# Kernel tuning notes

Measured on AMD Instinct MI355X. Metric: run time of the kernel, lower is better.

The kernel has to match this reference:

```python
import math
import jax, jax.numpy as jnp
import numpy as np

B, K, D, R = 8192, 64, 128, 8
EPSILON = 1.0  # alpha_scale, used as diffusion epsilon


def setup_inputs() -> dict:
    key = jax.random.key(0)
    k1, k2, k3 = jax.random.split(key, 3)
    y = jax.random.normal(k1, (B, D), dtype=jnp.float32)
    m = 0.2 * jax.random.normal(k2, (K, D), dtype=jnp.float32)          # init_mean_scale=0.2
    delta = jnp.full((K, D), -2.0, dtype=jnp.float32)                    # init_delta=-2.0
    U = 0.001 * jax.random.normal(k3, (K, D, R), dtype=jnp.float32)
    # log_alpha_raw = alpha_scale * log(ones(K)/K)
    log_alpha_raw = jnp.full((K,), math.log(1.0 / K), dtype=jnp.float32)
    return {"y": y, "m": m, "delta": delta, "U": U, "log_alpha_raw": log_alpha_raw}


def reference(y, m, delta, U, log_alpha_raw):
    """log z_theta(y) = logsumexp_k [log_alpha_k + log N(y; m_k, eps*S_k)],
    S_k = diag(exp(delta_k)) + U_k U_k^T, solved via Woodbury + Cholesky."""
    d = y.shape[-1]
    eps = jnp.asarray(EPSILON, y.dtype)
    log_alpha = (log_alpha_raw - jnp.mean(log_alpha_raw)) / EPSILON

    S_diag = jnp.exp(delta)            # [K, d]
    S_inv = 1.0 / S_diag               # [K, d]

    # Capacitance M_k = I_r + U_k^T diag(S_inv_k) U_k, Cholesky L_k
    V = S_inv[..., None] * U                              # [K, d, r]
    Mcap = jnp.eye(R, dtype=y.dtype) + jnp.einsum('kdr,kds->krs', U, V)  # [K, r, r]
    L = jnp.linalg.cholesky(Mcap)                         # [K, r, r]
    logdet_S = jnp.sum(jnp.log(S_diag), axis=-1) \
        + 2.0 * jnp.sum(jnp.log(jnp.diagonal(L, axis1=-2, axis2=-1)), axis=-1)  # [K]

    diff = y[:, None, :] - m[None, :, :]                  # [B, K, d]
    u1 = diff * S_inv[None]                               # [B, K, d]
    # Woodbury correction: solve M_k s = U_k^T u1 for all (b, k)
    t = jnp.einsum('kdr,bkd->krb', U, u1)                 # [K, r, B] (B as multiple RHS)
    z1 = jax.scipy.linalg.solve_triangular(L, t, lower=True)
    s = jax.scipy.linalg.solve_triangular(jnp.swapaxes(L, -1, -2), z1, lower=False)  # [K, r, B]
    Us = jnp.einsum('kdr,krb->bkd', U, s)                 # [B, K, d]
    S_inv_diff = u1 - Us * S_inv[None]                    # [B, K, d]

    quad = jnp.sum(diff * S_inv_diff, axis=-1)            # [B, K]
    log_norm = 0.5 * (d * (math.log(2.0 * math.pi) + jnp.log(eps)) + logdet_S)  # [K]
    logits = log_alpha[None, :] - 0.5 * quad / eps - log_norm[None, :]          # [B, K]
    return jax.scipy.special.logsumexp(logits, axis=-1)   # [B]
```

## Files before the change

kernel.cpp:

```cpp
#include <hip/hip_runtime.h>
#include <math.h>

#define D_DIM 128
#define K_DIM 64
#define R_DIM 8
#define B_DIM 8192
#define KG    4
#define XSTR  264
#define ESTR  161
#define TCH   5120

#define WS_C0F   81920
#define WS_PARTF 81984

typedef __bf16 bf16x8 __attribute__((ext_vector_type(8)));
typedef float  f32x4  __attribute__((ext_vector_type(4)));

static __device__ inline unsigned short f2bf(float f) {
  union { float f; unsigned int u; } v; v.f = f;
  unsigned int u = v.u;
  unsigned int lsb = (u >> 16) & 1;
  u += 0x7fffu + lsb;
  return (unsigned short)(u >> 16);
}

__global__ __launch_bounds__(128) void precomp_kernel(
    const float* __restrict__ m, const float* __restrict__ delta,
    const float* __restrict__ U, const float* __restrict__ lar,
    float* __restrict__ ws) {
  const int k = blockIdx.x;
  const int d = threadIdx.x;

  __shared__ float U_l[D_DIM][R_DIM];
  __shared__ float V_l[D_DIM][R_DIM];
  __shared__ float W_l[D_DIM][R_DIM];
  __shared__ float m_l[D_DIM];
  __shared__ float red[64];
  __shared__ float Linv_s[R_DIM][R_DIM];
  __shared__ float q_s[R_DIM];
  __shared__ float c0_s[1];
  __shared__ float redA[D_DIM], redB[D_DIM], redC[D_DIM];

  const float dl    = delta[k * D_DIM + d];
  const float s_inv = expf(-dl);
  const float mv    = m[k * D_DIM + d];
  m_l[d] = mv;
  const float* Up = U + (size_t)(k * D_DIM + d) * R_DIM;
#pragma unroll
  for (int r = 0; r < R_DIM; ++r) {
    float u = Up[r];
    U_l[d][r] = u;
    V_l[d][r] = u * s_inv;
  }
  redA[d] = dl;
  redB[d] = mv * mv * s_inv;
  redC[d] = (d < K_DIM) ? lar[d] : 0.f;
  __syncthreads();

  if (d < 64) {
    const int r = d >> 3, s = d & 7;
    float acc = (r == s) ? 1.0f : 0.0f;
#pragma unroll 8
    for (int dd = 0; dd < D_DIM; ++dd) acc += U_l[dd][r] * V_l[dd][s];
    red[d] = acc;
  }
  __syncthreads();

  for (int off = 64; off > 0; off >>= 1) {
    if (d < off) {
      redA[d] += redA[d + off];
      redB[d] += redB[d + off];
      redC[d] += redC[d + off];
    }
    __syncthreads();
  }

  if (d == 0) {
    float Lm[8][8];
#pragma unroll
    for (int i = 0; i < 8; ++i) {
#pragma unroll
      for (int j = 0; j < 8; ++j) {
        if (j > i) continue;
        float sum = red[i * 8 + j];
#pragma unroll
        for (int p = 0; p < 8; ++p)
          if (p < j) sum -= Lm[i][p] * Lm[j][p];
        if (i == j) Lm[i][i] = sqrtf(sum);
        else        Lm[i][j] = sum / Lm[j][j];
      }
    }
    float ld = 0.f;
#pragma unroll
    for (int i = 0; i < 8; ++i) ld += logf(Lm[i][i]);

    float Li[8][8];
#pragma unroll
    for (int i = 0; i < 8; ++i)
#pragma unroll
      for (int j = 0; j < 8; ++j) Li[i][j] = 0.f;
#pragma unroll
    for (int j = 0; j < 8; ++j) {
      Li[j][j] = 1.0f / Lm[j][j];
#pragma unroll
      for (int i = 0; i < 8; ++i) {
        if (i <= j) continue;
        float sum = 0.f;
#pragma unroll
        for (int p = 0; p < 8; ++p)
          if (p >= j && p < i) sum += Lm[i][p] * Li[p][j];
        Li[i][j] = -sum / Lm[i][i];
      }
    }
#pragma unroll
    for (int i = 0; i < 8; ++i)
#pragma unroll
      for (int j = 0; j < 8; ++j) Linv_s[i][j] = Li[i][j];

    const float mean = redC[0] * (1.0f / K_DIM);
    const float log_alpha = lar[k] - mean;
    const float logdetS = redA[0] + 2.0f * ld;
    const float LOG2PI = 1.8378770664093453f;
    const float log_norm = 0.5f * ((float)D_DIM * LOG2PI + logdetS);
    c0_s[0] = log_alpha - log_norm - 0.5f * redB[0];
  }
  __syncthreads();

  float Wr[R_DIM];
#pragma unroll
  for (int r = 0; r < R_DIM; ++r) {
    float acc = 0.f;
#pragma unroll
    for (int s2 = 0; s2 < R_DIM; ++s2)
      if (s2 <= r) acc += V_l[d][s2] * Linv_s[r][s2];
    Wr[r] = acc;
    W_l[d][r] = acc;
  }
  __syncthreads();

  if (d < R_DIM) {
    float acc = 0.f;
#pragma unroll 8
    for (int dd = 0; dd < D_DIM; ++dd) acc += W_l[dd][d] * m_l[dd];
    q_s[d] = acc;
  }
  __syncthreads();

  float hp = mv * s_inv;
#pragma unroll
  for (int r = 0; r < R_DIM; ++r) hp -= q_s[r] * Wr[r];

  const float INV_SQRT2 = 0.70710678118654752f;
  unsigned short* T = (unsigned short*)ws;
  const int kg = k >> 4, kl = k & 15;
  const int chunk = d >> 5, pos = d & 31;
  const size_t base_y = (((size_t)kg * 8 + chunk) * 160) * 32;
  const size_t base_q = (((size_t)kg * 8 + 4 + chunk) * 160) * 32;
#pragma unroll
  for (int c = 0; c < 8; ++c) {
    T[base_y + (size_t)(kl * 10 + c) * 32 + pos] = f2bf(Wr[c] * INV_SQRT2);
    T[base_q + (size_t)(kl * 10 + c) * 32 + pos] = 0;
  }
  T[base_y + (size_t)(kl * 10 + 8) * 32 + pos] = f2bf(hp);
  T[base_q + (size_t)(kl * 10 + 8) * 32 + pos] = f2bf(-0.5f * s_inv);
  T[base_y + (size_t)(kl * 10 + 9) * 32 + pos] = 0;
  T[base_q + (size_t)(kl * 10 + 9) * 32 + pos] = 0;

  if (d == 0) {
    float qq = 0.f;
#pragma unroll
    for (int r = 0; r < R_DIM; ++r) qq += q_s[r] * q_s[r];
    ws[WS_C0F + k] = c0_s[0] + 0.5f * qq;
  }
}

__global__ __launch_bounds__(256, 4) void logz_main(
    const float* __restrict__ y, const float* __restrict__ ws,
    float* __restrict__ part) {
  __shared__ __align__(16) unsigned short sX[32 * XSTR];
  __shared__ __align__(16) float sbuf[32 * ESTR];
  __shared__ float vals2[32 * 17];

  const int tid   = threadIdx.x;
  const int lane  = tid & 63;
  const int wv    = tid >> 6;
  const int wr    = wv >> 1;
  const int wc    = wv & 1;
  const int col_l = lane & 15;
  const int quad  = lane >> 4;
  const int rt    = (int)blockIdx.x >> 2;
  const int kg    = (int)blockIdx.x & 3;

  {
    const float4* yb = (const float4*)(y + (size_t)rt * 32 * D_DIM);
#pragma unroll
    for (int j = 0; j < 4; ++j) {
      const int idx = tid + j * 256;
      const int row = idx >> 5, seg = idx & 31;
      const float4 v = yb[idx];
      unsigned short* px = sX + row * XSTR + seg * 4;
      px[0] = f2bf(v.x); px[1] = f2bf(v.y);
      px[2] = f2bf(v.z); px[3] = f2bf(v.w);
      unsigned short* pq = px + 128;
      pq[0] = f2bf(v.x * v.x); pq[1] = f2bf(v.y * v.y);
      pq[2] = f2bf(v.z * v.z); pq[3] = f2bf(v.w * v.w);
    }
  }

  f32x4 acc[5];
#pragma unroll
  for (int f = 0; f < 5; ++f) { acc[f][0] = 0.f; acc[f][1] = 0.f; acc[f][2] = 0.f; acc[f][3] = 0.f; }

  const float* tG = ws + (size_t)kg * 8 * (TCH / 2);
  unsigned short* sT = (unsigned short*)sbuf;

  for (int pair = 0; pair < 4; ++pair) {
    __syncthreads();
    {
      const float* src = tG + (size_t)pair * TCH;
#pragma unroll
      for (int j = 0; j < 5; ++j) {
        const int off = (wv * 5 + j) * 256;
        __builtin_amdgcn_global_load_lds(
            (const __attribute__((address_space(1))) void*)(src + off + lane * 4),
            (__attribute__((address_space(3))) void*)((float*)sbuf + off),
            16, 0, 0);
      }
    }
    __syncthreads();
#pragma unroll
    for (int ii = 0; ii < 2; ++ii) {
      const int kiter = pair * 2 + ii;
      const bf16x8 a = *(const bf16x8*)(sX + (wr * 16 + col_l) * XSTR
                                          + kiter * 32 + quad * 8);
      const unsigned short* cb = sT + ii * TCH;
#pragma unroll
      for (int f = 0; f < 5; ++f) {
        const bf16x8 b = *(const bf16x8*)(cb + (wc * 80 + f * 16 + col_l) * 32
                                             + quad * 8);
        acc[f] = __builtin_amdgcn_mfma_f32_16x16x32_bf16(a, b, acc[f], 0, 0, 0);
      }
    }
  }

  __syncthreads();
  float* evals = sbuf;
#pragma unroll
  for (int f = 0; f < 5; ++f) {
    const int col = wc * 80 + f * 16 + col_l;
    const int c10 = col % 10;
#pragma unroll
    for (int reg = 0; reg < 4; ++reg) {
      const float v = acc[f][reg];
      evals[(wr * 16 + quad * 4 + reg) * ESTR + col] = (c10 == 8) ? v : v * v;
    }
  }
  __syncthreads();

  const float* c0p = ws + WS_C0F + kg * 16;
#pragma unroll
  for (int j = 0; j < 2; ++j) {
    const int idx = tid + j * 256;
    const int row = idx >> 4, kl = idx & 15;
    const float* e = evals + row * ESTR + kl * 10;
    float s = c0p[kl] + e[8];
#pragma unroll
    for (int c = 0; c < 8; ++c) s += e[c];
    vals2[row * 17 + kl] = s;
  }
  __syncthreads();

  if (tid < 32) {
    const int row = tid;
    float mx = -INFINITY;
#pragma unroll
    for (int j = 0; j < 16; ++j) mx = fmaxf(mx, vals2[row * 17 + j]);
    float s = 0.f;
#pragma unroll
    for (int j = 0; j < 16; ++j) s += expf(vals2[row * 17 + j] - mx);
    *(float2*)(part + ((size_t)(rt * 32 + row) * KG + kg) * 2) = make_float2(mx, s);
  }
}

__global__ __launch_bounds__(256) void reduce_kernel(
    const float* __restrict__ part, float* __restrict__ out) {
  const int b = blockIdx.x * 256 + threadIdx.x;
  const float4 a0 = ((const float4*)part)[b * 2];
  const float4 a1 = ((const float4*)part)[b * 2 + 1];
  float mx = fmaxf(fmaxf(a0.x, a0.z), fmaxf(a1.x, a1.z));
  float s = a0.y * expf(a0.x - mx) + a0.w * expf(a0.z - mx)
          + a1.y * expf(a1.x - mx) + a1.w * expf(a1.z - mx);
  out[b] = mx + logf(s);
}

extern "C" void kernel_launch(void* const* d_in, const int* in_sizes, int n_in,
                              void* d_out, int out_size, void* d_ws, size_t ws_size,
                              hipStream_t stream) {
  const float* y     = (const float*)d_in[0];
  const float* m     = (const float*)d_in[1];
  const float* delta = (const float*)d_in[2];
  const float* U     = (const float*)d_in[3];
  const float* lar   = (const float*)d_in[4];
  float* out = (float*)d_out;
  float* ws  = (float*)d_ws;

  precomp_kernel<<<K_DIM, 128, 0, stream>>>(m, delta, U, lar, ws);
  logz_main<<<(B_DIM / 32) * KG, 256, 0, stream>>>(y, ws, ws + WS_PARTF);
  reduce_kernel<<<B_DIM / 256, 256, 0, stream>>>(ws + WS_PARTF, out);
}
```

Measured before the change: 81.54 us.

## Precompute bf16 y and y^2 tiles in a prep kernel with XOR-swizzled layout

```diff
diff --git a/kernel.cpp b/kernel.cpp
--- a/kernel.cpp
+++ b/kernel.cpp
@@ -6,12 +6,12 @@
 #define R_DIM 8
 #define B_DIM 8192
 #define KG    4
-#define XSTR  264
 #define ESTR  161
 #define TCH   5120
 
 #define WS_C0F   81920
 #define WS_PARTF 81984
+#define WS_XGF   147520
 
 typedef __bf16 bf16x8 __attribute__((ext_vector_type(8)));
 typedef float  f32x4  __attribute__((ext_vector_type(4)));
@@ -174,10 +174,27 @@
   }
 }
 
+__global__ __launch_bounds__(256) void x_prep_kernel(
+    const float* __restrict__ y, float* __restrict__ ws) {
+  const int i   = blockIdx.x * 256 + threadIdx.x;
+  const int row = i >> 5;
+  const int seg = i & 31;
+  const float4* ya = (const float4*)y + (size_t)row * 32 + (seg & 15) * 2;
+  float4 a = ya[0], b = ya[1];
+  if (seg >= 16) {
+    a.x *= a.x; a.y *= a.y; a.z *= a.z; a.w *= a.w;
+    b.x *= b.x; b.y *= b.y; b.z *= b.z; b.w *= b.w;
+  }
+  union { unsigned short us[8]; uint4 v; } o;
+  o.us[0] = f2bf(a.x); o.us[1] = f2bf(a.y); o.us[2] = f2bf(a.z); o.us[3] = f2bf(a.w);
+  o.us[4] = f2bf(b.x); o.us[5] = f2bf(b.y); o.us[6] = f2bf(b.z); o.us[7] = f2bf(b.w);
+  uint4* xg = (uint4*)(ws + WS_XGF);
+  xg[(size_t)row * 32 + (seg ^ (row & 31))] = o.v;
+}
+
 __global__ __launch_bounds__(256, 4) void logz_main(
-    const float* __restrict__ y, const float* __restrict__ ws,
-    float* __restrict__ part) {
-  __shared__ __align__(16) unsigned short sX[32 * XSTR];
+    const float* __restrict__ ws, float* __restrict__ part) {
+  __shared__ __align__(16) unsigned short sX[32 * 256];
   __shared__ __align__(16) float sbuf[32 * ESTR];
   __shared__ float vals2[32 * 17];
 
@@ -192,18 +209,14 @@
   const int kg    = (int)blockIdx.x & 3;
 
   {
-    const float4* yb = (const float4*)(y + (size_t)rt * 32 * D_DIM);
+    const float* xsrc = ws + WS_XGF + (size_t)rt * 4096;
 #pragma unroll
     for (int j = 0; j < 4; ++j) {
-      const int idx = tid + j * 256;
-      const int row = idx >> 5, seg = idx & 31;
-      const float4 v = yb[idx];
-      unsigned short* px = sX + row * XSTR + seg * 4;
-      px[0] = f2bf(v.x); px[1] = f2bf(v.y);
-      px[2] = f2bf(v.z); px[3] = f2bf(v.w);
-      unsigned short* pq = px + 128;
-      pq[0] = f2bf(v.x * v.x); pq[1] = f2bf(v.y * v.y);
-      pq[2] = f2bf(v.z * v.z); pq[3] = f2bf(v.w * v.w);
+      const int off = (wv * 4 + j) * 256;
+      __builtin_amdgcn_global_load_lds(
+          (const __attribute__((address_space(1))) void*)(xsrc + off + lane * 4),
+          (__attribute__((address_space(3))) void*)((float*)sX + off),
+          16, 0, 0);
     }
   }
 
@@ -213,9 +226,10 @@
 
   const float* tG = ws + (size_t)kg * 8 * (TCH / 2);
   unsigned short* sT = (unsigned short*)sbuf;
+  const int rowA = wr * 16 + col_l;
 
   for (int pair = 0; pair < 4; ++pair) {
-    __syncthreads();
+    if (pair) __syncthreads();
     {
       const float* src = tG + (size_t)pair * TCH;
 #pragma unroll
@@ -231,8 +245,8 @@
 #pragma unroll
     for (int ii = 0; ii < 2; ++ii) {
       const int kiter = pair * 2 + ii;
-      const bf16x8 a = *(const bf16x8*)(sX + (wr * 16 + col_l) * XSTR
-                                          + kiter * 32 + quad * 8);
+      const bf16x8 a = *(const bf16x8*)(sX + ((size_t)rowA * 32
+                          + (((kiter * 4 + quad) ^ rowA) & 31)) * 8);
       const unsigned short* cb = sT + ii * TCH;
 #pragma unroll
       for (int f = 0; f < 5; ++f) {
@@ -305,6 +319,7 @@
   float* ws  = (float*)d_ws;
 
   precomp_kernel<<<K_DIM, 128, 0, stream>>>(m, delta, U, lar, ws);
-  logz_main<<<(B_DIM / 32) * KG, 256, 0, stream>>>(y, ws, ws + WS_PARTF);
+  x_prep_kernel<<<B_DIM * 32 / 256, 256, 0, stream>>>(y, ws);
+  logz_main<<<(B_DIM / 32) * KG, 256, 0, stream>>>(ws, ws + WS_PARTF);
   reduce_kernel<<<B_DIM / 256, 256, 0, stream>>>(ws + WS_PARTF, out);
 }
```

New measurement: 84.81 us. 4.0% more time.
